# Kernel tuning notes

Hardware: AMD Instinct MI355X
Metric: run time of the kernel (lower is better)

The kernel has to match this reference:

```python
import jax, jax.numpy as jnp
import numpy as np

NUM_HEADS = 16
EMB_DIM = 1024
HEAD_DIM = EMB_DIM // NUM_HEADS


def setup_inputs() -> dict:
    key = jax.random.key(0)
    k1, k2, k3, k4 = jax.random.split(key, 4)
    B, S = 2, 2048
    X = jax.random.normal(k1, (B, S, EMB_DIM), dtype=jnp.float32)
    # torch Linear(in, out, bias=False): y = x @ W.T ; store as [in, out]
    Wq = jax.random.normal(k2, (EMB_DIM, EMB_DIM), dtype=jnp.float32) * (EMB_DIM ** -0.5)
    Wk = jax.random.normal(k3, (EMB_DIM, HEAD_DIM), dtype=jnp.float32) * (EMB_DIM ** -0.5)
    Wv = jax.random.normal(k4, (EMB_DIM, HEAD_DIM), dtype=jnp.float32) * (EMB_DIM ** -0.5)
    return {"X": X, "Wq": Wq, "Wk": Wk, "Wv": Wv}


def reference(X, Wq, Wk, Wv):
    B, S, E = X.shape
    H, D = NUM_HEADS, HEAD_DIM
    q = (X @ Wq).reshape(B, S, H, D).transpose(0, 2, 1, 3)  # [B,H,S,D]
    k = X @ Wk  # [B,S,D] shared K head
    v = X @ Wv  # [B,S,D] shared V head
    scores = jnp.einsum('bhsd,btd->bhst', q, k) / jnp.sqrt(jnp.float32(D))
    causal = jnp.tril(jnp.ones((S, S), dtype=bool))
    scores = jnp.where(causal, scores, -jnp.inf)
    probs = jax.nn.softmax(scores, axis=-1)  # [B,H,S,S]
    out = jnp.einsum('bhst,btd->bhsd', probs, v)  # [B,H,S,D]
    return out.transpose(0, 2, 1, 3).reshape(B, S, E)
```

## Files before the change

### kernel.cpp

```cpp
#include <hip/hip_runtime.h>
#include <stdint.h>

#define NH   16
#define EMB  1024
#define HD   64
#define BSZ  2
#define SEQ  2048
#define NROW (BSZ * SEQ)

typedef __attribute__((ext_vector_type(8))) short bf16x8;
typedef __attribute__((ext_vector_type(4))) float f32x4;

__device__ __forceinline__ uint16_t f2bf(float f) {
    union { float f; uint32_t i; } v; v.f = f;
    uint32_t r = v.i + 0x7FFFu + ((v.i >> 16) & 1u);
    return (uint16_t)(r >> 16);
}
__device__ __forceinline__ uint32_t pack2(float a, float b) {
    return (uint32_t)f2bf(a) | ((uint32_t)f2bf(b) << 16);
}
__device__ __forceinline__ uint32_t cvtpk(float a, float b) {
    uint32_t r;
    asm("v_cvt_pk_bf16_f32 %0, %1, %2" : "=v"(r) : "v"(a), "v"(b));
    return r;
}

__device__ __forceinline__ void gl2lds16(const uint16_t* g, uint16_t* l) {
    __builtin_amdgcn_global_load_lds(
        static_cast<const uint32_t*>(static_cast<const void*>(g)),
        static_cast<uint32_t*>(static_cast<void*>(l)), 16, 0, 0);
}

__global__ __launch_bounds__(256) void prep(
    const float* __restrict__ X, uint16_t* __restrict__ Xbf,
    const float* __restrict__ Wq, const float* __restrict__ Wk,
    const float* __restrict__ Wv, uint16_t* __restrict__ Wqt,
    uint16_t* __restrict__ Wkt, uint16_t* __restrict__ Wvt)
{
    __shared__ uint16_t T[64][72];
    const int tid = threadIdx.x;
    if (blockIdx.x < 2048) {
        size_t idx = ((size_t)blockIdx.x * 256 + tid) * 8;
        float4 a = *(const float4*)&X[idx];
        float4 b = *(const float4*)&X[idx + 4];
        *(uint4*)&Xbf[idx] = make_uint4(pack2(a.x, a.y), pack2(a.z, a.w),
                                        pack2(b.x, b.y), pack2(b.z, b.w));
        return;
    }
    const int id = blockIdx.x - 2048;
    const float* W; uint16_t* Wt; int k0, n0, ldw;
    if (id < 256)      { W = Wq; Wt = Wqt; k0 = (id >> 4) * 64; n0 = (id & 15) * 64; ldw = EMB; }
    else if (id < 272) { W = Wk; Wt = Wkt; k0 = (id - 256) * 64; n0 = 0; ldw = HD; }
    else               { W = Wv; Wt = Wvt; k0 = (id - 272) * 64; n0 = 0; ldw = HD; }

    const int r = tid >> 2, c4 = (tid & 3) * 16;
#pragma unroll
    for (int i = 0; i < 4; ++i) {
        float4 wv = *(const float4*)&W[(size_t)(k0 + r) * ldw + n0 + c4 + 4 * i];
        T[r][c4 + 4 * i + 0] = f2bf(wv.x); T[r][c4 + 4 * i + 1] = f2bf(wv.y);
        T[r][c4 + 4 * i + 2] = f2bf(wv.z); T[r][c4 + 4 * i + 3] = f2bf(wv.w);
    }
    __syncthreads();
    const int n = tid >> 2, kk = (tid & 3) * 16;
    uint32_t o[8];
#pragma unroll
    for (int i = 0; i < 8; ++i)
        o[i] = (uint32_t)T[kk + 2 * i][n] | ((uint32_t)T[kk + 2 * i + 1][n] << 16);
    uint16_t* dst = &Wt[(size_t)(n0 + n) * EMB + k0 + kk];
    *(uint4*)dst       = make_uint4(o[0], o[1], o[2], o[3]);
    *(uint4*)(dst + 8) = make_uint4(o[4], o[5], o[6], o[7]);
}

__global__ __launch_bounds__(256) void qkv_gemm_mfma4(
    const uint16_t* __restrict__ Xbf, const uint16_t* __restrict__ Wqt,
    const uint16_t* __restrict__ Wkt, const uint16_t* __restrict__ Wvt,
    float* __restrict__ Qout, uint16_t* __restrict__ Kbf,
    uint16_t* __restrict__ Vtbf)
{
    const int tid  = threadIdx.x;
    const int w    = tid >> 6, lane = tid & 63;
    const int l    = lane & 15, quad = lane >> 4;
    const int wm   = w & 1, wn = w >> 1;
    const int nt   = blockIdx.x;
    const int m0   = blockIdx.y * 128;

    __shared__ uint16_t As[2][128 * 32];
    __shared__ uint16_t Bs[2][128 * 32];

    const uint16_t* gA[2]; uint32_t ldsA[2];
    const uint16_t* gB[2]; uint32_t ldsB[2];
#pragma unroll
    for (int i = 0; i < 2; ++i) {
        int ch = (w * 2 + i) * 64 + lane;
        int r = ch >> 2, cp = ch & 3;
        int c = cp ^ ((r >> 1) & 3);
        gA[i] = &Xbf[(size_t)(m0 + r) * EMB + c * 8];
        ldsA[i] = (w * 2 + i) * 512;
        const uint16_t* bs;
        if (nt < 8)      bs = &Wqt[(size_t)(nt * 128 + r) * EMB + c * 8];
        else if (r < 64) bs = &Wkt[(size_t)r * EMB + c * 8];
        else             bs = &Wvt[(size_t)(r - 64) * EMB + c * 8];
        gB[i] = bs;
        ldsB[i] = (w * 2 + i) * 512;
    }

    uint32_t offA[4], offB[4];
#pragma unroll
    for (int i = 0; i < 4; ++i) {
        int row = 64 * wm + 16 * i + l;
        offA[i] = (row * 4 + (quad ^ ((row >> 1) & 3))) * 8;
    }
#pragma unroll
    for (int j = 0; j < 4; ++j) {
        int row = 64 * wn + 16 * j + l;
        offB[j] = (row * 4 + (quad ^ ((row >> 1) & 3))) * 8;
    }

    f32x4 acc[4][4] = {};

    gl2lds16(gA[0], &As[0][ldsA[0]]);
    gl2lds16(gA[1], &As[0][ldsA[1]]);
    gl2lds16(gB[0], &Bs[0][ldsB[0]]);
    gl2lds16(gB[1], &Bs[0][ldsB[1]]);
    gA[0] += 32; gA[1] += 32; gB[0] += 32; gB[1] += 32;
    __syncthreads();

    for (int ks = 0; ks < 32; ++ks) {
        const int cur = ks & 1, nxt = cur ^ 1;
        if (ks < 31) {
            gl2lds16(gA[0], &As[nxt][ldsA[0]]);
            gl2lds16(gA[1], &As[nxt][ldsA[1]]);
            gl2lds16(gB[0], &Bs[nxt][ldsB[0]]);
            gl2lds16(gB[1], &Bs[nxt][ldsB[1]]);
            gA[0] += 32; gA[1] += 32; gB[0] += 32; gB[1] += 32;
        }
        bf16x8 af[4], bf[4];
#pragma unroll
        for (int i = 0; i < 4; ++i) af[i] = *(const bf16x8*)&As[cur][offA[i]];
#pragma unroll
        for (int j = 0; j < 4; ++j) bf[j] = *(const bf16x8*)&Bs[cur][offB[j]];
#pragma unroll
        for (int i = 0; i < 4; ++i)
#pragma unroll
            for (int j = 0; j < 4; ++j)
                acc[i][j] = __builtin_amdgcn_mfma_f32_16x16x32_bf16(
                    af[i], bf[j], acc[i][j], 0, 0, 0);
        __syncthreads();
    }

    if (nt < 8) {
#pragma unroll
        for (int i = 0; i < 4; ++i)
#pragma unroll
            for (int j = 0; j < 4; ++j)
#pragma unroll
                for (int r = 0; r < 4; ++r)
                    Qout[(size_t)(m0 + 64 * wm + 16 * i + 4 * quad + r) * EMB
                         + nt * 128 + 64 * wn + 16 * j + l] = acc[i][j][r];
    } else if (wn == 0) {
#pragma unroll
        for (int i = 0; i < 4; ++i)
#pragma unroll
            for (int j = 0; j < 4; ++j)
#pragma unroll
                for (int r = 0; r < 4; ++r)
                    Kbf[(size_t)(m0 + 64 * wm + 16 * i + 4 * quad + r) * HD
                        + 16 * j + l] = f2bf(acc[i][j][r]);
    } else {
#pragma unroll
        for (int i = 0; i < 4; ++i)
#pragma unroll
            for (int j = 0; j < 4; ++j)
#pragma unroll
                for (int r = 0; r < 4; ++r)
                    Vtbf[(size_t)(16 * j + l) * NROW
                         + m0 + 64 * wm + 16 * i + 4 * quad + r] = f2bf(acc[i][j][r]);
    }
}

__global__ __launch_bounds__(256) void mqa_attn(
    const uint16_t* __restrict__ Kbf, const uint16_t* __restrict__ Vtbf,
    float* __restrict__ Out)
{
    const int tid  = threadIdx.x;
    const int w    = tid >> 6;
    const int lane = tid & 63;
    const int l    = lane & 15;
    const int quad = lane >> 4;
    const int i  = blockIdx.x;
    const int h  = blockIdx.y, b = blockIdx.z;
    const int qt[2] = {31 - i, i};
    const int q0[2] = {qt[0] * 64, qt[1] * 64};

    __shared__ __align__(16) uint16_t KV[2][2][64][72];
    __shared__ __align__(16) uint16_t Ps[2][64][72];

    const float C = 0.125f * 1.4426950408889634f;
    const int sr = tid >> 2, sc = (tid & 3) * 16;

#pragma unroll
    for (int t = 0; t < 2; ++t) {
        const float* src = &Out[(size_t)(b * SEQ + q0[t] + sr) * EMB + h * HD + sc];
        float4 f0 = *(const float4*)(src + 0);
        float4 f1 = *(const float4*)(src + 4);
        float4 f2 = *(const float4*)(src + 8);
        float4 f3 = *(const float4*)(src + 12);
        *(uint4*)&Ps[t][sr][sc] =
            make_uint4(pack2(f0.x * C, f0.y * C), pack2(f0.z * C, f0.w * C),
                       pack2(f1.x * C, f1.y * C), pack2(f1.z * C, f1.w * C));
        *(uint4*)&Ps[t][sr][sc + 8] =
            make_uint4(pack2(f2.x * C, f2.y * C), pack2(f2.z * C, f2.w * C),
                       pack2(f3.x * C, f3.y * C), pack2(f3.z * C, f3.w * C));
    }

    uint4 kg0, kg1, vg0, vg1;
    {
        const uint4* ks = (const uint4*)&Kbf[(size_t)(b * SEQ + sr) * HD + sc];
        kg0 = ks[0]; kg1 = ks[1];
        const uint4* vs = (const uint4*)&Vtbf[(size_t)sr * NROW + b * SEQ + sc];
        vg0 = vs[0]; vg1 = vs[1];
    }
    *(uint4*)&KV[0][0][sr][sc]     = kg0;
    *(uint4*)&KV[0][0][sr][sc + 8] = kg1;
    *(uint4*)&KV[0][1][sr][sc]     = vg0;
    *(uint4*)&KV[0][1][sr][sc + 8] = vg1;
    {
        const uint4* ks = (const uint4*)&Kbf[(size_t)(b * SEQ + 64 + sr) * HD + sc];
        kg0 = ks[0]; kg1 = ks[1];
        const uint4* vs = (const uint4*)&Vtbf[(size_t)sr * NROW + b * SEQ + 64 + sc];
        vg0 = vs[0]; vg1 = vs[1];
    }
    __syncthreads();

    bf16x8 qf[2][2];
#pragma unroll
    for (int t = 0; t < 2; ++t) {
        qf[t][0] = *(const bf16x8*)&Ps[t][16 * w + l][quad * 8];
        qf[t][1] = *(const bf16x8*)&Ps[t][16 * w + l][32 + quad * 8];
    }

    bf16x8 ones;
#pragma unroll
    for (int j = 0; j < 8; ++j) ones[j] = (short)0x3F80;

    f32x4 accO[2][4] = {};
    f32x4 accSum[2] = {};
    const int qi_l = 16 * w + l;

    for (int kb = 0; kb <= qt[0]; ++kb) {
        const int cur = kb & 1, nxt = cur ^ 1;

        bf16x8 ka[4][2];
#pragma unroll
        for (int ts = 0; ts < 4; ++ts) {
            ka[ts][0] = *(const bf16x8*)&KV[cur][0][16 * ts + l][quad * 8];
            ka[ts][1] = *(const bf16x8*)&KV[cur][0][16 * ts + l][32 + quad * 8];
        }

        if (kb < qt[0]) {
            *(uint4*)&KV[nxt][0][sr][sc]     = kg0;
            *(uint4*)&KV[nxt][0][sr][sc + 8] = kg1;
            *(uint4*)&KV[nxt][1][sr][sc]     = vg0;
            *(uint4*)&KV[nxt][1][sr][sc + 8] = vg1;
            if (kb + 1 < qt[0]) {
                const int k0n = (kb + 2) * 64;
                const uint4* ks = (const uint4*)&Kbf[(size_t)(b * SEQ + k0n + sr) * HD + sc];
                kg0 = ks[0]; kg1 = ks[1];
                const uint4* vs = (const uint4*)&Vtbf[(size_t)sr * NROW + b * SEQ + k0n + sc];
                vg0 = vs[0]; vg1 = vs[1];
            }
        }

        const bool doB = (kb <= qt[1]);

#pragma unroll
        for (int t = 0; t < 2; ++t) {
            if (t == 1 && !doB) break;
            f32x4 accS[4] = {};
#pragma unroll
            for (int ts = 0; ts < 4; ++ts) {
                accS[ts] = __builtin_amdgcn_mfma_f32_16x16x32_bf16(ka[ts][0], qf[t][0], accS[ts], 0, 0, 0);
                accS[ts] = __builtin_amdgcn_mfma_f32_16x16x32_bf16(ka[ts][1], qf[t][1], accS[ts], 0, 0, 0);
            }
            float pv[16];
#pragma unroll
            for (int ts = 0; ts < 4; ++ts)
#pragma unroll
                for (int r = 0; r < 4; ++r)
                    pv[4 * ts + r] = exp2f(accS[ts][r]);
            if (kb == qt[t]) {
#pragma unroll
                for (int ts = 0; ts < 4; ++ts)
#pragma unroll
                    for (int r = 0; r < 4; ++r)
                        if ((16 * ts + 4 * quad + r) > qi_l) pv[4 * ts + r] = 0.f;
            }
#pragma unroll
            for (int ts = 0; ts < 4; ++ts)
                *(uint2*)&Ps[t][16 * w + l][16 * ts + 4 * quad] =
                    make_uint2(cvtpk(pv[4 * ts + 0], pv[4 * ts + 1]),
                               cvtpk(pv[4 * ts + 2], pv[4 * ts + 3]));
        }

        bf16x8 vb[4][2];
#pragma unroll
        for (int tn = 0; tn < 4; ++tn) {
            vb[tn][0] = *(const bf16x8*)&KV[cur][1][16 * tn + l][quad * 8];
            vb[tn][1] = *(const bf16x8*)&KV[cur][1][16 * tn + l][32 + quad * 8];
        }
#pragma unroll
        for (int t = 0; t < 2; ++t) {
            if (t == 1 && !doB) break;
            bf16x8 pa0 = *(const bf16x8*)&Ps[t][16 * w + l][quad * 8];
            bf16x8 pa1 = *(const bf16x8*)&Ps[t][16 * w + l][32 + quad * 8];
#pragma unroll
            for (int tn = 0; tn < 4; ++tn) {
                accO[t][tn] = __builtin_amdgcn_mfma_f32_16x16x32_bf16(pa0, vb[tn][0], accO[t][tn], 0, 0, 0);
                accO[t][tn] = __builtin_amdgcn_mfma_f32_16x16x32_bf16(pa1, vb[tn][1], accO[t][tn], 0, 0, 0);
            }
            accSum[t] = __builtin_amdgcn_mfma_f32_16x16x32_bf16(pa0, ones, accSum[t], 0, 0, 0);
            accSum[t] = __builtin_amdgcn_mfma_f32_16x16x32_bf16(pa1, ones, accSum[t], 0, 0, 0);
        }

        __syncthreads();
    }

#pragma unroll
    for (int t = 0; t < 2; ++t) {
#pragma unroll
        for (int r = 0; r < 4; ++r) {
            float invr = 1.0f / accSum[t][r];
            const int row = q0[t] + 16 * w + 4 * quad + r;
#pragma unroll
            for (int tn = 0; tn < 4; ++tn)
                Out[(size_t)(b * SEQ + row) * EMB + h * HD + 16 * tn + l] =
                    accO[t][tn][r] * invr;
        }
    }
}

__global__ __launch_bounds__(256) void qkv_gemm_vec(
    const float* __restrict__ X,  const float* __restrict__ Wq,
    const float* __restrict__ Wk, const float* __restrict__ Wv,
    float* __restrict__ Qout, uint16_t* __restrict__ Kbf,
    uint16_t* __restrict__ Vtbf)
{
    const int tid = threadIdx.x;
    const int tx = tid & 15, ty = tid >> 4;
    const int bx = blockIdx.x;
    const int m0 = blockIdx.y * 64;

    const float* W; int ldw, n0;
    if (bx < 16)       { W = Wq; ldw = EMB; n0 = bx * 64; }
    else if (bx == 16) { W = Wk; ldw = HD;  n0 = 0; }
    else               { W = Wv; ldw = HD;  n0 = 0; }

    __shared__ float sA[64][17];
    __shared__ float sB[16][64];

    float acc[4][4] = {};
    const int arow = tid >> 2, acol = (tid & 3) * 4;
    const int brow = tid >> 4, bcol = (tid & 15) * 4;

    for (int k0 = 0; k0 < EMB; k0 += 16) {
        float4 fa = *(const float4*)&X[(size_t)(m0 + arow) * EMB + k0 + acol];
        float4 fb = *(const float4*)&W[(size_t)(k0 + brow) * ldw + n0 + bcol];
        sA[arow][acol + 0] = fa.x; sA[arow][acol + 1] = fa.y;
        sA[arow][acol + 2] = fa.z; sA[arow][acol + 3] = fa.w;
        sB[brow][bcol + 0] = fb.x; sB[brow][bcol + 1] = fb.y;
        sB[brow][bcol + 2] = fb.z; sB[brow][bcol + 3] = fb.w;
        __syncthreads();
#pragma unroll
        for (int kk = 0; kk < 16; ++kk) {
            float a0 = sA[4 * ty + 0][kk];
            float a1 = sA[4 * ty + 1][kk];
            float a2 = sA[4 * ty + 2][kk];
            float a3 = sA[4 * ty + 3][kk];
            float4 bq = *(const float4*)&sB[kk][4 * tx];
            acc[0][0] += a0 * bq.x; acc[0][1] += a0 * bq.y; acc[0][2] += a0 * bq.z; acc[0][3] += a0 * bq.w;
            acc[1][0] += a1 * bq.x; acc[1][1] += a1 * bq.y; acc[1][2] += a1 * bq.z; acc[1][3] += a1 * bq.w;
            acc[2][0] += a2 * bq.x; acc[2][1] += a2 * bq.y; acc[2][2] += a2 * bq.z; acc[2][3] += a2 * bq.w;
            acc[3][0] += a3 * bq.x; acc[3][1] += a3 * bq.y; acc[3][2] += a3 * bq.z; acc[3][3] += a3 * bq.w;
        }
        __syncthreads();
    }

    if (bx < 16) {
#pragma unroll
        for (int i = 0; i < 4; ++i)
            *(float4*)&Qout[(size_t)(m0 + 4 * ty + i) * EMB + n0 + 4 * tx] =
                make_float4(acc[i][0], acc[i][1], acc[i][2], acc[i][3]);
    } else if (bx == 16) {
#pragma unroll
        for (int i = 0; i < 4; ++i) {
            ushort4 u; u.x = f2bf(acc[i][0]); u.y = f2bf(acc[i][1]);
            u.z = f2bf(acc[i][2]); u.w = f2bf(acc[i][3]);
            *(ushort4*)&Kbf[(size_t)(m0 + 4 * ty + i) * HD + 4 * tx] = u;
        }
    } else {
#pragma unroll
        for (int j = 0; j < 4; ++j) {
            ushort4 u; u.x = f2bf(acc[0][j]); u.y = f2bf(acc[1][j]);
            u.z = f2bf(acc[2][j]); u.w = f2bf(acc[3][j]);
            *(ushort4*)&Vtbf[(size_t)(4 * tx + j) * NROW + m0 + 4 * ty] = u;
        }
    }
}

extern "C" void kernel_launch(void* const* d_in, const int* in_sizes, int n_in,
                              void* d_out, int out_size, void* d_ws, size_t ws_size,
                              hipStream_t stream) {
    const float* X  = (const float*)d_in[0];
    const float* Wq = (const float*)d_in[1];
    const float* Wk = (const float*)d_in[2];
    const float* Wv = (const float*)d_in[3];
    float* OutP = (float*)d_out;

    char* ws = (char*)d_ws;
    const size_t MB = 1024 * 1024;
    uint16_t* Xbf  = (uint16_t*)(ws);
    uint16_t* Wqt  = (uint16_t*)(ws + 8 * MB);
    uint16_t* Wkt  = (uint16_t*)(ws + 10 * MB);
    uint16_t* Wvt  = (uint16_t*)(ws + 10 * MB + 256 * 1024);
    uint16_t* Kbf  = (uint16_t*)(ws + 10 * MB + 512 * 1024);
    uint16_t* Vtbf = (uint16_t*)(ws + 11 * MB);

    if (ws_size >= 12 * MB) {
        prep<<<2336, 256, 0, stream>>>(X, Xbf, Wq, Wk, Wv, Wqt, Wkt, Wvt);
        qkv_gemm_mfma4<<<dim3(9, 32), 256, 0, stream>>>(Xbf, Wqt, Wkt, Wvt,
                                                        OutP, Kbf, Vtbf);
        mqa_attn<<<dim3(16, NH, BSZ), 256, 0, stream>>>(Kbf, Vtbf, OutP);
    } else {
        uint16_t* KbfS  = (uint16_t*)d_ws;
        uint16_t* VtbfS = KbfS + (size_t)NROW * HD;
        qkv_gemm_vec<<<dim3(18, 64), 256, 0, stream>>>(X, Wq, Wk, Wv, OutP, KbfS, VtbfS);
        mqa_attn<<<dim3(16, NH, BSZ), 256, 0, stream>>>(KbfS, VtbfS, OutP);
    }
}
```

Before: 150.4 us.

## Retile QKV GEMM to 64x128 with K=64 steps; specialize attention loop phases

```diff
diff --git a/kernel.cpp b/kernel.cpp
--- a/kernel.cpp
+++ b/kernel.cpp
@@ -71,7 +71,7 @@
     *(uint4*)(dst + 8) = make_uint4(o[4], o[5], o[6], o[7]);
 }
 
-__global__ __launch_bounds__(256) void qkv_gemm_mfma4(
+__global__ __launch_bounds__(256) void qkv_gemm_mfma5(
     const uint16_t* __restrict__ Xbf, const uint16_t* __restrict__ Wqt,
     const uint16_t* __restrict__ Wkt, const uint16_t* __restrict__ Wvt,
     float* __restrict__ Qout, uint16_t* __restrict__ Kbf,
@@ -82,99 +82,108 @@
     const int l    = lane & 15, quad = lane >> 4;
     const int wm   = w & 1, wn = w >> 1;
     const int nt   = blockIdx.x;
-    const int m0   = blockIdx.y * 128;
-
-    __shared__ uint16_t As[2][128 * 32];
-    __shared__ uint16_t Bs[2][128 * 32];
+    const int m0   = blockIdx.y * 64;
+
+    __shared__ uint16_t As[2][64 * 64];
+    __shared__ uint16_t Bs[2][128 * 64];
 
     const uint16_t* gA[2]; uint32_t ldsA[2];
-    const uint16_t* gB[2]; uint32_t ldsB[2];
+    const uint16_t* gB[4]; uint32_t ldsB[4];
 #pragma unroll
     for (int i = 0; i < 2; ++i) {
-        int ch = (w * 2 + i) * 64 + lane;
-        int r = ch >> 2, cp = ch & 3;
-        int c = cp ^ ((r >> 1) & 3);
-        gA[i] = &Xbf[(size_t)(m0 + r) * EMB + c * 8];
+        int G = (w * 2 + i) * 64 + lane;
+        int r = G >> 3, cg = (G & 7) ^ (r & 7);
+        gA[i] = &Xbf[(size_t)(m0 + r) * EMB + cg * 8];
         ldsA[i] = (w * 2 + i) * 512;
+    }
+#pragma unroll
+    for (int i = 0; i < 4; ++i) {
+        int G = (w * 4 + i) * 64 + lane;
+        int r = G >> 3, cg = (G & 7) ^ (r & 7);
         const uint16_t* bs;
-        if (nt < 8)      bs = &Wqt[(size_t)(nt * 128 + r) * EMB + c * 8];
-        else if (r < 64) bs = &Wkt[(size_t)r * EMB + c * 8];
-        else             bs = &Wvt[(size_t)(r - 64) * EMB + c * 8];
+        if (nt < 8)      bs = &Wqt[(size_t)(nt * 128 + r) * EMB + cg * 8];
+        else if (r < 64) bs = &Wkt[(size_t)r * EMB + cg * 8];
+        else             bs = &Wvt[(size_t)(r - 64) * EMB + cg * 8];
         gB[i] = bs;
-        ldsB[i] = (w * 2 + i) * 512;
-    }
-
-    uint32_t offA[4], offB[4];
-#pragma unroll
-    for (int i = 0; i < 4; ++i) {
-        int row = 64 * wm + 16 * i + l;
-        offA[i] = (row * 4 + (quad ^ ((row >> 1) & 3))) * 8;
-    }
-#pragma unroll
-    for (int j = 0; j < 4; ++j) {
-        int row = 64 * wn + 16 * j + l;
-        offB[j] = (row * 4 + (quad ^ ((row >> 1) & 3))) * 8;
-    }
-
-    f32x4 acc[4][4] = {};
-
-    gl2lds16(gA[0], &As[0][ldsA[0]]);
-    gl2lds16(gA[1], &As[0][ldsA[1]]);
-    gl2lds16(gB[0], &Bs[0][ldsB[0]]);
-    gl2lds16(gB[1], &Bs[0][ldsB[1]]);
-    gA[0] += 32; gA[1] += 32; gB[0] += 32; gB[1] += 32;
+        ldsB[i] = (w * 4 + i) * 512;
+    }
+
+    uint32_t offA[2][2], offB[4][2];
+#pragma unroll
+    for (int i = 0; i < 2; ++i)
+#pragma unroll
+        for (int kh = 0; kh < 2; ++kh) {
+            int row = 32 * wm + 16 * i + l;
+            offA[i][kh] = row * 64 + (((kh * 4 + quad) ^ (row & 7)) * 8);
+        }
+#pragma unroll
+    for (int j = 0; j < 4; ++j)
+#pragma unroll
+        for (int kh = 0; kh < 2; ++kh) {
+            int row = 64 * wn + 16 * j + l;
+            offB[j][kh] = row * 64 + (((kh * 4 + quad) ^ (row & 7)) * 8);
+        }
+
+    f32x4 acc[2][4] = {};
+
+#pragma unroll
+    for (int i = 0; i < 2; ++i) { gl2lds16(gA[i], &As[0][ldsA[i]]); gA[i] += 64; }
+#pragma unroll
+    for (int i = 0; i < 4; ++i) { gl2lds16(gB[i], &Bs[0][ldsB[i]]); gB[i] += 64; }
     __syncthreads();
 
-    for (int ks = 0; ks < 32; ++ks) {
+    for (int ks = 0; ks < 16; ++ks) {
         const int cur = ks & 1, nxt = cur ^ 1;
-        if (ks < 31) {
-            gl2lds16(gA[0], &As[nxt][ldsA[0]]);
-            gl2lds16(gA[1], &As[nxt][ldsA[1]]);
-            gl2lds16(gB[0], &Bs[nxt][ldsB[0]]);
-            gl2lds16(gB[1], &Bs[nxt][ldsB[1]]);
-            gA[0] += 32; gA[1] += 32; gB[0] += 32; gB[1] += 32;
-        }
-        bf16x8 af[4], bf[4];
-#pragma unroll
-        for (int i = 0; i < 4; ++i) af[i] = *(const bf16x8*)&As[cur][offA[i]];
-#pragma unroll
-        for (int j = 0; j < 4; ++j) bf[j] = *(const bf16x8*)&Bs[cur][offB[j]];
-#pragma unroll
-        for (int i = 0; i < 4; ++i)
+        if (ks < 15) {
+#pragma unroll
+            for (int i = 0; i < 2; ++i) { gl2lds16(gA[i], &As[nxt][ldsA[i]]); gA[i] += 64; }
+#pragma unroll
+            for (int i = 0; i < 4; ++i) { gl2lds16(gB[i], &Bs[nxt][ldsB[i]]); gB[i] += 64; }
+        }
+#pragma unroll
+        for (int kh = 0; kh < 2; ++kh) {
+            bf16x8 af[2], bfr[4];
+#pragma unroll
+            for (int i = 0; i < 2; ++i) af[i] = *(const bf16x8*)&As[cur][offA[i][kh]];
+#pragma unroll
+            for (int j = 0; j < 4; ++j) bfr[j] = *(const bf16x8*)&Bs[cur][offB[j][kh]];
+#pragma unroll
+            for (int i = 0; i < 2; ++i)
+#pragma unroll
+                for (int j = 0; j < 4; ++j)
+                    acc[i][j] = __builtin_amdgcn_mfma_f32_16x16x32_bf16(
+                        af[i], bfr[j], acc[i][j], 0, 0, 0);
+        }
+        __syncthreads();
+    }
+
+    if (nt < 8) {
+#pragma unroll
+        for (int i = 0; i < 2; ++i)
 #pragma unroll
             for (int j = 0; j < 4; ++j)
-                acc[i][j] = __builtin_amdgcn_mfma_f32_16x16x32_bf16(
-                    af[i], bf[j], acc[i][j], 0, 0, 0);
-        __syncthreads();
-    }
-
-    if (nt < 8) {
-#pragma unroll
-        for (int i = 0; i < 4; ++i)
-#pragma unroll
-            for (int j = 0; j < 4; ++j)
 #pragma unroll
                 for (int r = 0; r < 4; ++r)
-                    Qout[(size_t)(m0 + 64 * wm + 16 * i + 4 * quad + r) * EMB
+                    Qout[(size_t)(m0 + 32 * wm + 16 * i + 4 * quad + r) * EMB
                          + nt * 128 + 64 * wn + 16 * j + l] = acc[i][j][r];
     } else if (wn == 0) {
 #pragma unroll
-        for (int i = 0; i < 4; ++i)
+        for (int i = 0; i < 2; ++i)
 #pragma unroll
             for (int j = 0; j < 4; ++j)
 #pragma unroll
                 for (int r = 0; r < 4; ++r)
-                    Kbf[(size_t)(m0 + 64 * wm + 16 * i + 4 * quad + r) * HD
+                    Kbf[(size_t)(m0 + 32 * wm + 16 * i + 4 * quad + r) * HD
                         + 16 * j + l] = f2bf(acc[i][j][r]);
     } else {
 #pragma unroll
-        for (int i = 0; i < 4; ++i)
+        for (int i = 0; i < 2; ++i)
 #pragma unroll
             for (int j = 0; j < 4; ++j)
 #pragma unroll
                 for (int r = 0; r < 4; ++r)
                     Vtbf[(size_t)(16 * j + l) * NROW
-                         + m0 + 64 * wm + 16 * i + 4 * quad + r] = f2bf(acc[i][j][r]);
+                         + m0 + 32 * wm + 16 * i + 4 * quad + r] = f2bf(acc[i][j][r]);
     }
 }
 
@@ -189,8 +198,8 @@
     const int quad = lane >> 4;
     const int i  = blockIdx.x;
     const int h  = blockIdx.y, b = blockIdx.z;
-    const int qt[2] = {31 - i, i};
-    const int q0[2] = {qt[0] * 64, qt[1] * 64};
+    const int qt0 = 31 - i, qt1 = i;
+    const int q00 = qt0 * 64, q01 = qt1 * 64;
 
     __shared__ __align__(16) uint16_t KV[2][2][64][72];
     __shared__ __align__(16) uint16_t Ps[2][64][72];
@@ -200,7 +209,8 @@
 
 #pragma unroll
     for (int t = 0; t < 2; ++t) {
-        const float* src = &Out[(size_t)(b * SEQ + q0[t] + sr) * EMB + h * HD + sc];
+        const int q0t = t ? q01 : q00;
+        const float* src = &Out[(size_t)(b * SEQ + q0t + sr) * EMB + h * HD + sc];
         float4 f0 = *(const float4*)(src + 0);
         float4 f1 = *(const float4*)(src + 4);
         float4 f2 = *(const float4*)(src + 8);
@@ -247,7 +257,7 @@
     f32x4 accSum[2] = {};
     const int qi_l = 16 * w + l;
 
-    for (int kb = 0; kb <= qt[0]; ++kb) {
+    auto body = [&](int kb, bool DO1, bool M0, bool M1) __attribute__((always_inline)) {
         const int cur = kb & 1, nxt = cur ^ 1;
 
         bf16x8 ka[4][2];
@@ -257,12 +267,12 @@
             ka[ts][1] = *(const bf16x8*)&KV[cur][0][16 * ts + l][32 + quad * 8];
         }
 
-        if (kb < qt[0]) {
+        if (kb < qt0) {
             *(uint4*)&KV[nxt][0][sr][sc]     = kg0;
             *(uint4*)&KV[nxt][0][sr][sc + 8] = kg1;
             *(uint4*)&KV[nxt][1][sr][sc]     = vg0;
             *(uint4*)&KV[nxt][1][sr][sc + 8] = vg1;
-            if (kb + 1 < qt[0]) {
+            if (kb + 1 < qt0) {
                 const int k0n = (kb + 2) * 64;
                 const uint4* ks = (const uint4*)&Kbf[(size_t)(b * SEQ + k0n + sr) * HD + sc];
                 kg0 = ks[0]; kg1 = ks[1];
@@ -271,24 +281,30 @@
             }
         }
 
-        const bool doB = (kb <= qt[1]);
-
-#pragma unroll
-        for (int t = 0; t < 2; ++t) {
-            if (t == 1 && !doB) break;
-            f32x4 accS[4] = {};
+        f32x4 accS0[4] = {}, accS1[4] = {};
+        __builtin_amdgcn_s_setprio(1);
+#pragma unroll
+        for (int ts = 0; ts < 4; ++ts) {
+            accS0[ts] = __builtin_amdgcn_mfma_f32_16x16x32_bf16(ka[ts][0], qf[0][0], accS0[ts], 0, 0, 0);
+            accS0[ts] = __builtin_amdgcn_mfma_f32_16x16x32_bf16(ka[ts][1], qf[0][1], accS0[ts], 0, 0, 0);
+        }
+        if (DO1) {
 #pragma unroll
             for (int ts = 0; ts < 4; ++ts) {
-                accS[ts] = __builtin_amdgcn_mfma_f32_16x16x32_bf16(ka[ts][0], qf[t][0], accS[ts], 0, 0, 0);
-                accS[ts] = __builtin_amdgcn_mfma_f32_16x16x32_bf16(ka[ts][1], qf[t][1], accS[ts], 0, 0, 0);
+                accS1[ts] = __builtin_amdgcn_mfma_f32_16x16x32_bf16(ka[ts][0], qf[1][0], accS1[ts], 0, 0, 0);
+                accS1[ts] = __builtin_amdgcn_mfma_f32_16x16x32_bf16(ka[ts][1], qf[1][1], accS1[ts], 0, 0, 0);
             }
+        }
+        __builtin_amdgcn_s_setprio(0);
+
+        {
             float pv[16];
 #pragma unroll
             for (int ts = 0; ts < 4; ++ts)
 #pragma unroll
                 for (int r = 0; r < 4; ++r)
-                    pv[4 * ts + r] = exp2f(accS[ts][r]);
-            if (kb == qt[t]) {
+                    pv[4 * ts + r] = exp2f(accS0[ts][r]);
+            if (M0) {
 #pragma unroll
                 for (int ts = 0; ts < 4; ++ts)
 #pragma unroll
@@ -297,7 +313,27 @@
             }
 #pragma unroll
             for (int ts = 0; ts < 4; ++ts)
-                *(uint2*)&Ps[t][16 * w + l][16 * ts + 4 * quad] =
+                *(uint2*)&Ps[0][16 * w + l][16 * ts + 4 * quad] =
+                    make_uint2(cvtpk(pv[4 * ts + 0], pv[4 * ts + 1]),
+                               cvtpk(pv[4 * ts + 2], pv[4 * ts + 3]));
+        }
+        if (DO1) {
+            float pv[16];
+#pragma unroll
+            for (int ts = 0; ts < 4; ++ts)
+#pragma unroll
+                for (int r = 0; r < 4; ++r)
+                    pv[4 * ts + r] = exp2f(accS1[ts][r]);
+            if (M1) {
+#pragma unroll
+                for (int ts = 0; ts < 4; ++ts)
+#pragma unroll
+                    for (int r = 0; r < 4; ++r)
+                        if ((16 * ts + 4 * quad + r) > qi_l) pv[4 * ts + r] = 0.f;
+            }
+#pragma unroll
+            for (int ts = 0; ts < 4; ++ts)
+                *(uint2*)&Ps[1][16 * w + l][16 * ts + 4 * quad] =
                     make_uint2(cvtpk(pv[4 * ts + 0], pv[4 * ts + 1]),
                                cvtpk(pv[4 * ts + 2], pv[4 * ts + 3]));
         }
@@ -308,29 +344,45 @@
             vb[tn][0] = *(const bf16x8*)&KV[cur][1][16 * tn + l][quad * 8];
             vb[tn][1] = *(const bf16x8*)&KV[cur][1][16 * tn + l][32 + quad * 8];
         }
-#pragma unroll
-        for (int t = 0; t < 2; ++t) {
-            if (t == 1 && !doB) break;
-            bf16x8 pa0 = *(const bf16x8*)&Ps[t][16 * w + l][quad * 8];
-            bf16x8 pa1 = *(const bf16x8*)&Ps[t][16 * w + l][32 + quad * 8];
+
+        bf16x8 pa00 = *(const bf16x8*)&Ps[0][16 * w + l][quad * 8];
+        bf16x8 pa01 = *(const bf16x8*)&Ps[0][16 * w + l][32 + quad * 8];
+        __builtin_amdgcn_s_setprio(1);
+#pragma unroll
+        for (int tn = 0; tn < 4; ++tn) {
+            accO[0][tn] = __builtin_amdgcn_mfma_f32_16x16x32_bf16(pa00, vb[tn][0], accO[0][tn], 0, 0, 0);
+            accO[0][tn] = __builtin_amdgcn_mfma_f32_16x16x32_bf16(pa01, vb[tn][1], accO[0][tn], 0, 0, 0);
+        }
+        accSum[0] = __builtin_amdgcn_mfma_f32_16x16x32_bf16(pa00, ones, accSum[0], 0, 0, 0);
+        accSum[0] = __builtin_amdgcn_mfma_f32_16x16x32_bf16(pa01, ones, accSum[0], 0, 0, 0);
+        if (DO1) {
+            bf16x8 pa10 = *(const bf16x8*)&Ps[1][16 * w + l][quad * 8];
+            bf16x8 pa11 = *(const bf16x8*)&Ps[1][16 * w + l][32 + quad * 8];
 #pragma unroll
             for (int tn = 0; tn < 4; ++tn) {
-                accO[t][tn] = __builtin_amdgcn_mfma_f32_16x16x32_bf16(pa0, vb[tn][0], accO[t][tn], 0, 0, 0);
-                accO[t][tn] = __builtin_amdgcn_mfma_f32_16x16x32_bf16(pa1, vb[tn][1], accO[t][tn], 0, 0, 0);
+                accO[1][tn] = __builtin_amdgcn_mfma_f32_16x16x32_bf16(pa10, vb[tn][0], accO[1][tn], 0, 0, 0);
+                accO[1][tn] = __builtin_amdgcn_mfma_f32_16x16x32_bf16(pa11, vb[tn][1], accO[1][tn], 0, 0, 0);
             }
-            accSum[t] = __builtin_amdgcn_mfma_f32_16x16x32_bf16(pa0, ones, accSum[t], 0, 0, 0);
-            accSum[t] = __builtin_amdgcn_mfma_f32_16x16x32_bf16(pa1, ones, accSum[t], 0, 0, 0);
-        }
+            accSum[1] = __builtin_amdgcn_mfma_f32_16x16x32_bf16(pa10, ones, accSum[1], 0, 0, 0);
+            accSum[1] = __builtin_amdgcn_mfma_f32_16x16x32_bf16(pa11, ones, accSum[1], 0, 0, 0);
+        }
+        __builtin_amdgcn_s_setprio(0);
 
         __syncthreads();
-    }
+    };
+
+    for (int kb = 0; kb < qt1; ++kb) body(kb, true,  false, false);
+    body(qt1, true,  false, true);
+    for (int kb = qt1 + 1; kb < qt0; ++kb) body(kb, false, false, false);
+    body(qt0, false, true,  false);
 
 #pragma unroll
     for (int t = 0; t < 2; ++t) {
+        const int q0t = t ? q01 : q00;
 #pragma unroll
         for (int r = 0; r < 4; ++r) {
             float invr = 1.0f / accSum[t][r];
-            const int row = q0[t] + 16 * w + 4 * quad + r;
+            const int row = q0t + 16 * w + 4 * quad + r;
 #pragma unroll
             for (int tn = 0; tn < 4; ++tn)
                 Out[(size_t)(b * SEQ + row) * EMB + h * HD + 16 * tn + l] =
@@ -427,7 +479,7 @@
 
     if (ws_size >= 12 * MB) {
         prep<<<2336, 256, 0, stream>>>(X, Xbf, Wq, Wk, Wv, Wqt, Wkt, Wvt);
-        qkv_gemm_mfma4<<<dim3(9, 32), 256, 0, stream>>>(Xbf, Wqt, Wkt, Wvt,
+        qkv_gemm_mfma5<<<dim3(9, 64), 256, 0, stream>>>(Xbf, Wqt, Wkt, Wvt,
                                                         OutP, Kbf, Vtbf);
         mqa_attn<<<dim3(16, NH, BSZ), 256, 0, stream>>>(Kbf, Vtbf, OutP);
     } else {
```

Measured after the change: 142.7 us. 5.2% less time.
